# Optimization experiments

Hardware: AMD Instinct MI355X
Metric: run time of the kernel (lower is better)

The kernel has to match this reference:

```python
import jax, jax.numpy as jnp
import numpy as np
import math

N, CI, H, W, D = 8, 64, 64, 64, 64  # batch, input_dim, spatial, d_model


def setup_inputs() -> dict:
    key = jax.random.key(0)
    ks = jax.random.split(key, 6)
    s = 0.05
    return {
        "h": jax.random.normal(ks[0], (N, CI, H, W), jnp.float32),
        "m": jax.random.normal(ks[1], (N, CI, H, W), jnp.float32),
        # conv_h: 1x1, input_dim -> 3*d_model
        "Wh": jax.random.normal(ks[2], (3 * D, CI), jnp.float32) * s,
        "bh": jnp.zeros((3 * D,), jnp.float32),
        # conv_m: 1x1, input_dim -> 2*d_model
        "Wm": jax.random.normal(ks[3], (2 * D, CI), jnp.float32) * s,
        "bm": jnp.zeros((2 * D,), jnp.float32),
        # conv_z: 1x1, 2*d_model -> d_model
        "Wz": jax.random.normal(ks[4], (D, 2 * D), jnp.float32) * s,
        "bz": jnp.zeros((D,), jnp.float32),
        # conv_output: 3x3, input_dim + d_model -> 3*input_dim
        "Wo": jax.random.normal(ks[5], (3 * CI, CI + D, 3, 3), jnp.float32) * s,
        "bo": jnp.zeros((3 * CI,), jnp.float32),
    }


def _conv1x1(x, Wt, b):
    # x: (N,C,H,W), Wt: (O,C)
    return jnp.einsum('nchw,oc->nohw', x, Wt) + b[None, :, None, None]


def _attn(q, k, v):
    # q,k,v: (N,C,S); softmax over key positions
    C = q.shape[1]
    scores = jnp.einsum('ncs,nct->nst', q, k) / math.sqrt(C)  # (N,S,S)
    a = jax.nn.softmax(scores, axis=-1)
    return jnp.einsum('nst,nct->ncs', a, v)  # (N,C,S)


def reference(h, m, Wh, bh, Wm, bm, Wz, bz, Wo, bo):
    n, _, hh, ww = h.shape
    hq, hk, hv = jnp.split(_conv1x1(h, Wh, bh), 3, axis=1)
    mk, mv = jnp.split(_conv1x1(m, Wm, bm), 2, axis=1)
    flat = lambda x: x.reshape(n, D, hh * ww)
    Zh = _attn(flat(hq), flat(hk), flat(hv))
    Zm = _attn(flat(hq), flat(mk), flat(mv))
    Zcat = jnp.concatenate([Zh.reshape(n, D, hh, ww), Zm.reshape(n, D, hh, ww)], axis=1)
    Z = _conv1x1(Zcat, Wz, bz)
    x = jnp.concatenate([Z, h], axis=1)  # (N, CI+D, H, W)
    y = jax.lax.conv_general_dilated(
        x, Wo, window_strides=(1, 1), padding='SAME',
        dimension_numbers=('NCHW', 'OIHW', 'NCHW')) + bo[None, :, None, None]
    i, g, o = jnp.split(y, 3, axis=1)
    i = jax.nn.sigmoid(i)
    g = jnp.tanh(g)
    m_next = i * g + (1.0 - i) * m
    h_next = jax.nn.sigmoid(o) * m_next
    return (h_next, m_next)
```

## Files before the change

### kernel.cpp

```cpp
#include <hip/hip_runtime.h>
#include <hip/hip_bf16.h>
#include <math.h>

typedef __attribute__((ext_vector_type(8))) short bf16x8;
typedef __attribute__((ext_vector_type(4))) float f32x4;

#define DEVI __device__ __forceinline__

DEVI unsigned short f2bf(float f) {
  unsigned int u = __builtin_bit_cast(unsigned int, f);
  unsigned int r = (u + 0x7fffu + ((u >> 16) & 1u)) >> 16;
  return (unsigned short)r;
}
DEVI float bf2f(unsigned int h) {
  unsigned int u = (h & 0xffffu) << 16;
  return __builtin_bit_cast(float, u);
}
DEVI float exp2v(float x) {
  float r;
  asm("v_exp_f32 %0, %1" : "=v"(r) : "v"(x));
  return r;
}

__global__ __launch_bounds__(256) void k_prep_wo(const float* __restrict__ Wo,
                                                 unsigned short* __restrict__ wo_t) {
  int i = blockIdx.x * 256 + threadIdx.x;
  if (i >= 9 * 192 * 128) return;
  int c = i & 127;
  int rem = i >> 7;
  int o = rem % 192;
  int dydx = rem / 192;
  wo_t[i] = f2bf(Wo[(o * 128 + c) * 9 + dydx]);
}

__global__ __launch_bounds__(256) void k_prep_h(const float* __restrict__ h,
                                                unsigned short* __restrict__ xcat) {
  int i = blockIdx.x * 256 + threadIdx.x;
  int base = i * 4;
  int n = base >> 18;
  int r = base & 262143;
  int c = r >> 12;
  int s = r & 4095;
  float4 v = *(const float4*)(h + base);
  unsigned short tmp[4] = {f2bf(v.x), f2bf(v.y), f2bf(v.z), f2bf(v.w)};
  *(unsigned long long*)(xcat + (((size_t)n * 128 + 64 + c) << 12) + s) =
      *(const unsigned long long*)tmp;
}

__global__ __launch_bounds__(256) void k_proj(
    const float* __restrict__ h, const float* __restrict__ m,
    const float* __restrict__ Wh, const float* __restrict__ bh,
    const float* __restrict__ Wm, const float* __restrict__ bm,
    unsigned short* __restrict__ qb, unsigned short* __restrict__ kb,
    unsigned short* __restrict__ kmb, unsigned short* __restrict__ vb,
    unsigned short* __restrict__ vmb) {
  __shared__ float xt[64][32];
  __shared__ float wt[64][68];
  const int t = threadIdx.x;
  const int st0 = blockIdx.x * 32;
  const int n = blockIdx.y;
  const int ob = blockIdx.z;
  const float* __restrict__ x = (ob < 3) ? h : m;
  const float* __restrict__ W = (ob < 3) ? Wh : Wm;
  const float* __restrict__ bias = (ob < 3) ? bh : bm;
  const int obase = (ob < 3) ? ob * 64 : (ob - 3) * 64;

  {
    const int s = t & 31, cq = t >> 5;
    const float* src = x + (((size_t)n * 64) << 12) + st0 + s;
    #pragma unroll
    for (int r = 0; r < 8; ++r) { int c = cq + 8 * r; xt[c][s] = src[(size_t)c << 12]; }
  }
  {
    const int c = t & 63, oq = t >> 6;
    #pragma unroll
    for (int r = 0; r < 16; ++r) {
      int o = oq + 4 * r;
      wt[c][o] = W[(size_t)(obase + o) * 64 + c];
    }
  }
  __syncthreads();

  if (ob == 0 || ob == 1 || ob == 3) {
    const int og = t & 7, s = t >> 3;
    float acc[8];
    #pragma unroll
    for (int k = 0; k < 8; ++k) acc[k] = bias[obase + og * 8 + k];
    for (int c = 0; c < 64; ++c) {
      const float xv = xt[c][s];
      const float4 wa = *(const float4*)&wt[c][og * 8];
      const float4 wb = *(const float4*)&wt[c][og * 8 + 4];
      acc[0] += wa.x * xv; acc[1] += wa.y * xv; acc[2] += wa.z * xv; acc[3] += wa.w * xv;
      acc[4] += wb.x * xv; acc[5] += wb.y * xv; acc[6] += wb.z * xv; acc[7] += wb.w * xv;
    }
    const float scale = (ob == 0) ? 0.125f * 1.44269504088896340736f : 1.0f;
    unsigned short* dst = (ob == 0) ? qb : (ob == 1 ? kb : kmb);
    unsigned short tmp[8];
    #pragma unroll
    for (int k = 0; k < 8; ++k) tmp[k] = f2bf(acc[k] * scale);
    *(uint4*)(dst + (((size_t)n * 4096 + st0 + s) << 6) + og * 8) = *(const uint4*)tmp;
  } else {
    const int o = t & 63, sg = t >> 6;
    float acc[8];
    const float bv = bias[obase + o];
    #pragma unroll
    for (int k = 0; k < 8; ++k) acc[k] = bv;
    for (int c = 0; c < 64; ++c) {
      const float wv = wt[c][o];
      #pragma unroll
      for (int u = 0; u < 8; ++u) acc[u] += wv * xt[c][sg * 8 + u];
    }
    unsigned short* dst = (ob == 2) ? vb : vmb;
    unsigned short tmp[8];
    #pragma unroll
    for (int k = 0; k < 8; ++k) tmp[k] = f2bf(acc[k]);
    *(uint4*)(dst + (((size_t)n * 64 + o) << 12) + st0 + sg * 8) = *(const uint4*)tmp;
  }
}

__global__ __launch_bounds__(256) void k_attn(
    const unsigned short* __restrict__ qb, const unsigned short* __restrict__ kb,
    const unsigned short* __restrict__ kmb, const unsigned short* __restrict__ vb,
    const unsigned short* __restrict__ vmb, unsigned short* __restrict__ zcat) {
  __shared__ unsigned short Pl[4][2048];
  const int t = threadIdx.x;
  const int w = t >> 6, l = t & 63;
  const int lg = l >> 4, ll = l & 15;
  const int qt = blockIdx.x, n = blockIdx.y, sel = blockIdx.z;
  const unsigned short* __restrict__ Ksrc = sel ? kmb : kb;
  const unsigned short* __restrict__ Vsrc = sel ? vmb : vb;

  const int qbase = qt * 128 + w * 32;
  bf16x8 qfA0, qfA1, qfB0, qfB1;
  {
    const unsigned short* qp = qb + (((size_t)n * 4096 + qbase + ll) << 6) + lg * 8;
    qfA0 = *(const bf16x8*)(qp);
    qfA1 = *(const bf16x8*)(qp + 32);
    qfB0 = *(const bf16x8*)(qp + 1024);
    qfB1 = *(const bf16x8*)(qp + 1056);
  }
  f32x4 OA[4], OB[4];
  #pragma unroll
  for (int ct = 0; ct < 4; ++ct)
    #pragma unroll
    for (int e = 0; e < 4; ++e) { OA[ct][e] = 0.f; OB[ct][e] = 0.f; }
  float lsA = 0.f, lsB = 0.f;

  const unsigned short* kp = Ksrc + ((size_t)n << 18) + ((size_t)ll << 6) + lg * 8;
  const unsigned short* vp = Vsrc + ((size_t)n << 18) + ((size_t)ll << 12) + lg * 8;
  char* PlB = (char*)&Pl[w][0];
  const int swz = (ll & 7) << 4;
  const int wb = ll * 128 + lg * 8;
  const int rb = ll * 128 + lg * 16;

  for (int kt = 0; kt < 64; ++kt) {
    bf16x8 kf[8], vf[8];
    #pragma unroll
    for (int ct = 0; ct < 4; ++ct) {
      #pragma unroll
      for (int k2 = 0; k2 < 2; ++k2) {
        kf[ct * 2 + k2] = *(const bf16x8*)(kp + kt * 4096 + ct * 1024 + k2 * 32);
        vf[ct * 2 + k2] = *(const bf16x8*)(vp + (ct << 16) + kt * 64 + k2 * 32);
      }
    }
    f32x4 scA[4], scB[4];
    #pragma unroll
    for (int ct = 0; ct < 4; ++ct)
      #pragma unroll
      for (int e = 0; e < 4; ++e) { scA[ct][e] = 0.f; scB[ct][e] = 0.f; }
    #pragma unroll
    for (int k2 = 0; k2 < 2; ++k2) {
      #pragma unroll
      for (int ct = 0; ct < 4; ++ct) {
        scA[ct] = __builtin_amdgcn_mfma_f32_16x16x32_bf16(kf[ct * 2 + k2],
                      k2 ? qfA1 : qfA0, scA[ct], 0, 0, 0);
        scB[ct] = __builtin_amdgcn_mfma_f32_16x16x32_bf16(kf[ct * 2 + k2],
                      k2 ? qfB1 : qfB0, scB[ct], 0, 0, 0);
      }
    }
    #pragma unroll
    for (int ct = 0; ct < 4; ++ct) {
      float a0 = exp2v(scA[ct][0]), a1 = exp2v(scA[ct][1]);
      float a2 = exp2v(scA[ct][2]), a3 = exp2v(scA[ct][3]);
      lsA += (a0 + a1) + (a2 + a3);
      unsigned int u0, u1;
      asm("v_cvt_pk_bf16_f32 %0, %1, %2" : "=v"(u0) : "v"(a0), "v"(a1));
      asm("v_cvt_pk_bf16_f32 %0, %1, %2" : "=v"(u1) : "v"(a2), "v"(a3));
      uint2 prA; prA.x = u0; prA.y = u1;
      *(uint2*)(PlB + ((wb + ct * 32) ^ swz)) = prA;
      float b0 = exp2v(scB[ct][0]), b1 = exp2v(scB[ct][1]);
      float b2 = exp2v(scB[ct][2]), b3 = exp2v(scB[ct][3]);
      lsB += (b0 + b1) + (b2 + b3);
      unsigned int u2, u3;
      asm("v_cvt_pk_bf16_f32 %0, %1, %2" : "=v"(u2) : "v"(b0), "v"(b1));
      asm("v_cvt_pk_bf16_f32 %0, %1, %2" : "=v"(u3) : "v"(b2), "v"(b3));
      uint2 prB; prB.x = u2; prB.y = u3;
      *(uint2*)(PlB + 2048 + ((wb + ct * 32) ^ swz)) = prB;
    }
    bf16x8 pa0 = *(const bf16x8*)(PlB + (rb ^ swz));
    bf16x8 pa1 = *(const bf16x8*)(PlB + ((rb + 64) ^ swz));
    bf16x8 pb0 = *(const bf16x8*)(PlB + 2048 + (rb ^ swz));
    bf16x8 pb1 = *(const bf16x8*)(PlB + 2048 + ((rb + 64) ^ swz));
    #pragma unroll
    for (int k2 = 0; k2 < 2; ++k2) {
      #pragma unroll
      for (int ct = 0; ct < 4; ++ct) {
        OA[ct] = __builtin_amdgcn_mfma_f32_16x16x32_bf16(k2 ? pa1 : pa0,
                     vf[ct * 2 + k2], OA[ct], 0, 0, 0);
        OB[ct] = __builtin_amdgcn_mfma_f32_16x16x32_bf16(k2 ? pb1 : pb0,
                     vf[ct * 2 + k2], OB[ct], 0, 0, 0);
      }
    }
  }
  lsA += __shfl_xor(lsA, 16); lsA += __shfl_xor(lsA, 32);
  lsB += __shfl_xor(lsB, 16); lsB += __shfl_xor(lsB, 32);
  #pragma unroll
  for (int r = 0; r < 4; ++r) {
    const float liA = 1.f / __shfl(lsA, lg * 4 + r);
    const float liB = 1.f / __shfl(lsB, lg * 4 + r);
    const int rowA = qbase + lg * 4 + r;
    #pragma unroll
    for (int ct = 0; ct < 4; ++ct) {
      const int c = sel * 64 + ct * 16 + ll;
      zcat[(((size_t)n * 4096 + rowA) << 7) + c] = f2bf(OA[ct][r] * liA);
      zcat[(((size_t)n * 4096 + rowA + 16) << 7) + c] = f2bf(OB[ct][r] * liB);
    }
  }
}

__global__ __launch_bounds__(256) void k_zgemm(
    const unsigned short* __restrict__ zcat, const float* __restrict__ Wz,
    const float* __restrict__ bz, unsigned short* __restrict__ xcat) {
  __shared__ float zt[32][132];
  __shared__ float wzt[128][68];
  const int t = threadIdx.x;
  const int st0 = blockIdx.x * 32, n = blockIdx.y;
  {
    #pragma unroll
    for (int r = 0; r < 2; ++r) {
      const int chunk = t + 256 * r;
      const int s = chunk >> 4, kp = chunk & 15;
      const uint4 d = *(const uint4*)(zcat + (((size_t)n * 4096 + st0 + s) << 7) + kp * 8);
      const unsigned int u[4] = {d.x, d.y, d.z, d.w};
      #pragma unroll
      for (int e = 0; e < 4; ++e) {
        zt[s][kp * 8 + 2 * e]     = bf2f(u[e]);
        zt[s][kp * 8 + 2 * e + 1] = bf2f(u[e] >> 16);
      }
    }
  }
  {
    const int k = t & 127, czq = t >> 7;
    #pragma unroll
    for (int r = 0; r < 32; ++r) {
      const int cz = czq + 2 * r;
      wzt[k][cz] = Wz[((size_t)cz << 7) + k];
    }
  }
  __syncthreads();
  const int cz = t & 63, sg = t >> 6;
  float acc[8];
  const float bv = bz[cz];
  #pragma unroll
  for (int u = 0; u < 8; ++u) acc[u] = bv;
  for (int k = 0; k < 128; ++k) {
    const float wv = wzt[k][cz];
    #pragma unroll
    for (int u = 0; u < 8; ++u) acc[u] += wv * zt[sg * 8 + u][k];
  }
  unsigned short tmp[8];
  #pragma unroll
  for (int u = 0; u < 8; ++u) tmp[u] = f2bf(acc[u]);
  *(uint4*)(xcat + (((size_t)n * 128 + cz) << 12) + st0 + sg * 8) = *(const uint4*)tmp;
}

__global__ __launch_bounds__(256) void k_conv(
    const unsigned short* __restrict__ xcat, const unsigned short* __restrict__ wo_t,
    const float* __restrict__ bo, const float* __restrict__ m_in,
    float* __restrict__ out) {
  __shared__ unsigned short xt[3][66][40];
  const int t = threadIdx.x;
  const int wv = t >> 6, l = t & 63, lg = l >> 4, ll = l & 15;
  const int y = blockIdx.x, n = blockIdx.y;
  f32x4 acc[3][4];
  #pragma unroll
  for (int ot = 0; ot < 3; ++ot)
    #pragma unroll
    for (int ct = 0; ct < 4; ++ct)
      #pragma unroll
      for (int e = 0; e < 4; ++e) acc[ot][ct][e] = 0.f;

  for (int cb = 0; cb < 4; ++cb) {
    __syncthreads();
    {
      if (t < 192) {
        const int side = t / 96, rr = t % 96;
        xt[rr >> 5][side * 65][rr & 31] = 0;
      }
      const int wx = t & 63, q = t >> 6;
      #pragma unroll
      for (int r = 0; r < 24; ++r) {
        const int idx = q + 4 * r;
        const int c = idx & 31, dy = idx >> 5;
        const int yin = y + dy - 1;
        unsigned short vv = 0;
        if (yin >= 0 && yin < 64)
          vv = xcat[(((size_t)n * 128 + cb * 32 + c) << 12) + yin * 64 + wx];
        xt[dy][wx + 1][c] = vv;
      }
    }
    __syncthreads();
    #pragma unroll
    for (int dy = 0; dy < 3; ++dy) {
      #pragma unroll
      for (int dx = 0; dx < 3; ++dx) {
        bf16x8 bfr[4];
        #pragma unroll
        for (int ct = 0; ct < 4; ++ct)
          bfr[ct] = *(const bf16x8*)&xt[dy][ct * 16 + ll + dx][lg * 8];
        #pragma unroll
        for (int ot = 0; ot < 3; ++ot) {
          const int o = (wv + ot * 4) * 16 + ll;
          const bf16x8 afr = *(const bf16x8*)(wo_t +
              (((size_t)(dy * 3 + dx) * 192 + o) << 7) + cb * 32 + lg * 8);
          #pragma unroll
          for (int ct = 0; ct < 4; ++ct)
            acc[ot][ct] = __builtin_amdgcn_mfma_f32_16x16x32_bf16(afr, bfr[ct], acc[ot][ct], 0, 0, 0);
        }
      }
    }
  }
  #pragma unroll
  for (int ct = 0; ct < 4; ++ct) {
    #pragma unroll
    for (int r = 0; r < 4; ++r) {
      const int c = wv * 16 + lg * 4 + r;
      const int sx = ct * 16 + ll;
      const size_t pix = (((size_t)n * 64 + c) << 12) + y * 64 + sx;
      const float yi = acc[0][ct][r] + bo[c];
      const float yg = acc[1][ct][r] + bo[64 + c];
      const float yo = acc[2][ct][r] + bo[128 + c];
      const float iv = 1.f / (1.f + __expf(-yi));
      const float gv = tanhf(yg);
      const float ov = 1.f / (1.f + __expf(-yo));
      const float mo = m_in[pix];
      const float mn = iv * gv + (1.f - iv) * mo;
      out[pix] = ov * mn;
      out[pix + 2097152] = mn;
    }
  }
}

extern "C" void kernel_launch(void* const* d_in, const int* in_sizes, int n_in,
                              void* d_out, int out_size, void* d_ws, size_t ws_size,
                              hipStream_t stream) {
  const float* h  = (const float*)d_in[0];
  const float* m  = (const float*)d_in[1];
  const float* Wh = (const float*)d_in[2];
  const float* bh = (const float*)d_in[3];
  const float* Wm = (const float*)d_in[4];
  const float* bm = (const float*)d_in[5];
  const float* Wz = (const float*)d_in[6];
  const float* bz = (const float*)d_in[7];
  const float* Wo = (const float*)d_in[8];
  const float* bo = (const float*)d_in[9];
  float* out = (float*)d_out;

  unsigned short* ws  = (unsigned short*)d_ws;
  unsigned short* qbf  = ws;
  unsigned short* kbf  = qbf + 2097152;
  unsigned short* kmbf = kbf + 2097152;
  unsigned short* vbf  = kmbf + 2097152;
  unsigned short* vmbf = vbf + 2097152;
  unsigned short* zcat = vmbf + 2097152;
  unsigned short* xcat = zcat + 4194304;
  unsigned short* wot  = xcat + 4194304;

  hipLaunchKernelGGL(k_prep_wo, dim3(864), dim3(256), 0, stream, Wo, wot);
  hipLaunchKernelGGL(k_prep_h, dim3(2048), dim3(256), 0, stream, h, xcat);
  hipLaunchKernelGGL(k_proj, dim3(128, 8, 5), dim3(256), 0, stream,
                     h, m, Wh, bh, Wm, bm, qbf, kbf, kmbf, vbf, vmbf);
  hipLaunchKernelGGL(k_attn, dim3(32, 8, 2), dim3(256), 0, stream,
                     qbf, kbf, kmbf, vbf, vmbf, zcat);
  hipLaunchKernelGGL(k_zgemm, dim3(128, 8), dim3(256), 0, stream, zcat, Wz, bz, xcat);
  hipLaunchKernelGGL(k_conv, dim3(64, 8), dim3(256), 0, stream, xcat, wot, bo, m, out);
}
```

Baseline: 421.7 us.

## Split attention work to 16 query rows per wave with 512-thread blocks

```diff
diff --git a/kernel.cpp b/kernel.cpp
--- a/kernel.cpp
+++ b/kernel.cpp
@@ -118,33 +118,35 @@
   }
 }
 
-__global__ __launch_bounds__(256) void k_attn(
+__global__ __launch_bounds__(512, 4) void k_attn(
     const unsigned short* __restrict__ qb, const unsigned short* __restrict__ kb,
     const unsigned short* __restrict__ kmb, const unsigned short* __restrict__ vb,
     const unsigned short* __restrict__ vmb, unsigned short* __restrict__ zcat) {
-  __shared__ unsigned short Pl[4][2048];
+  __shared__ unsigned short Pl[8][1024];
   const int t = threadIdx.x;
   const int w = t >> 6, l = t & 63;
   const int lg = l >> 4, ll = l & 15;
-  const int qt = blockIdx.x, n = blockIdx.y, sel = blockIdx.z;
+  const int bid = blockIdx.x;
+  const int n = bid & 7;
+  const int r0 = bid >> 3;
+  const int sel = r0 & 1;
+  const int qt = r0 >> 1;
   const unsigned short* __restrict__ Ksrc = sel ? kmb : kb;
   const unsigned short* __restrict__ Vsrc = sel ? vmb : vb;
 
-  const int qbase = qt * 128 + w * 32;
-  bf16x8 qfA0, qfA1, qfB0, qfB1;
+  const int qbase = qt * 128 + w * 16;
+  bf16x8 qf0, qf1;
   {
     const unsigned short* qp = qb + (((size_t)n * 4096 + qbase + ll) << 6) + lg * 8;
-    qfA0 = *(const bf16x8*)(qp);
-    qfA1 = *(const bf16x8*)(qp + 32);
-    qfB0 = *(const bf16x8*)(qp + 1024);
-    qfB1 = *(const bf16x8*)(qp + 1056);
-  }
-  f32x4 OA[4], OB[4];
+    qf0 = *(const bf16x8*)(qp);
+    qf1 = *(const bf16x8*)(qp + 32);
+  }
+  f32x4 OA[4];
   #pragma unroll
   for (int ct = 0; ct < 4; ++ct)
     #pragma unroll
-    for (int e = 0; e < 4; ++e) { OA[ct][e] = 0.f; OB[ct][e] = 0.f; }
-  float lsA = 0.f, lsB = 0.f;
+    for (int e = 0; e < 4; ++e) OA[ct][e] = 0.f;
+  float lsA = 0.f;
 
   const unsigned short* kp = Ksrc + ((size_t)n << 18) + ((size_t)ll << 6) + lg * 8;
   const unsigned short* vp = Vsrc + ((size_t)n << 18) + ((size_t)ll << 12) + lg * 8;
@@ -163,67 +165,50 @@
         vf[ct * 2 + k2] = *(const bf16x8*)(vp + (ct << 16) + kt * 64 + k2 * 32);
       }
     }
-    f32x4 scA[4], scB[4];
+    f32x4 sc[4];
     #pragma unroll
     for (int ct = 0; ct < 4; ++ct)
       #pragma unroll
-      for (int e = 0; e < 4; ++e) { scA[ct][e] = 0.f; scB[ct][e] = 0.f; }
+      for (int e = 0; e < 4; ++e) sc[ct][e] = 0.f;
     #pragma unroll
     for (int k2 = 0; k2 < 2; ++k2) {
       #pragma unroll
       for (int ct = 0; ct < 4; ++ct) {
-        scA[ct] = __builtin_amdgcn_mfma_f32_16x16x32_bf16(kf[ct * 2 + k2],
-                      k2 ? qfA1 : qfA0, scA[ct], 0, 0, 0);
-        scB[ct] = __builtin_amdgcn_mfma_f32_16x16x32_bf16(kf[ct * 2 + k2],
-                      k2 ? qfB1 : qfB0, scB[ct], 0, 0, 0);
+        sc[ct] = __builtin_amdgcn_mfma_f32_16x16x32_bf16(kf[ct * 2 + k2],
+                     k2 ? qf1 : qf0, sc[ct], 0, 0, 0);
       }
     }
     #pragma unroll
     for (int ct = 0; ct < 4; ++ct) {
-      float a0 = exp2v(scA[ct][0]), a1 = exp2v(scA[ct][1]);
-      float a2 = exp2v(scA[ct][2]), a3 = exp2v(scA[ct][3]);
+      float a0 = exp2v(sc[ct][0]), a1 = exp2v(sc[ct][1]);
+      float a2 = exp2v(sc[ct][2]), a3 = exp2v(sc[ct][3]);
       lsA += (a0 + a1) + (a2 + a3);
       unsigned int u0, u1;
       asm("v_cvt_pk_bf16_f32 %0, %1, %2" : "=v"(u0) : "v"(a0), "v"(a1));
       asm("v_cvt_pk_bf16_f32 %0, %1, %2" : "=v"(u1) : "v"(a2), "v"(a3));
-      uint2 prA; prA.x = u0; prA.y = u1;
-      *(uint2*)(PlB + ((wb + ct * 32) ^ swz)) = prA;
-      float b0 = exp2v(scB[ct][0]), b1 = exp2v(scB[ct][1]);
-      float b2 = exp2v(scB[ct][2]), b3 = exp2v(scB[ct][3]);
-      lsB += (b0 + b1) + (b2 + b3);
-      unsigned int u2, u3;
-      asm("v_cvt_pk_bf16_f32 %0, %1, %2" : "=v"(u2) : "v"(b0), "v"(b1));
-      asm("v_cvt_pk_bf16_f32 %0, %1, %2" : "=v"(u3) : "v"(b2), "v"(b3));
-      uint2 prB; prB.x = u2; prB.y = u3;
-      *(uint2*)(PlB + 2048 + ((wb + ct * 32) ^ swz)) = prB;
+      uint2 pr; pr.x = u0; pr.y = u1;
+      *(uint2*)(PlB + ((wb + ct * 32) ^ swz)) = pr;
     }
     bf16x8 pa0 = *(const bf16x8*)(PlB + (rb ^ swz));
     bf16x8 pa1 = *(const bf16x8*)(PlB + ((rb + 64) ^ swz));
-    bf16x8 pb0 = *(const bf16x8*)(PlB + 2048 + (rb ^ swz));
-    bf16x8 pb1 = *(const bf16x8*)(PlB + 2048 + ((rb + 64) ^ swz));
     #pragma unroll
     for (int k2 = 0; k2 < 2; ++k2) {
       #pragma unroll
       for (int ct = 0; ct < 4; ++ct) {
         OA[ct] = __builtin_amdgcn_mfma_f32_16x16x32_bf16(k2 ? pa1 : pa0,
                      vf[ct * 2 + k2], OA[ct], 0, 0, 0);
-        OB[ct] = __builtin_amdgcn_mfma_f32_16x16x32_bf16(k2 ? pb1 : pb0,
-                     vf[ct * 2 + k2], OB[ct], 0, 0, 0);
       }
     }
   }
   lsA += __shfl_xor(lsA, 16); lsA += __shfl_xor(lsA, 32);
-  lsB += __shfl_xor(lsB, 16); lsB += __shfl_xor(lsB, 32);
   #pragma unroll
   for (int r = 0; r < 4; ++r) {
     const float liA = 1.f / __shfl(lsA, lg * 4 + r);
-    const float liB = 1.f / __shfl(lsB, lg * 4 + r);
     const int rowA = qbase + lg * 4 + r;
     #pragma unroll
     for (int ct = 0; ct < 4; ++ct) {
       const int c = sel * 64 + ct * 16 + ll;
       zcat[(((size_t)n * 4096 + rowA) << 7) + c] = f2bf(OA[ct][r] * liA);
-      zcat[(((size_t)n * 4096 + rowA + 16) << 7) + c] = f2bf(OB[ct][r] * liB);
     }
   }
 }
@@ -380,7 +365,7 @@
   hipLaunchKernelGGL(k_prep_h, dim3(2048), dim3(256), 0, stream, h, xcat);
   hipLaunchKernelGGL(k_proj, dim3(128, 8, 5), dim3(256), 0, stream,
                      h, m, Wh, bh, Wm, bm, qbf, kbf, kmbf, vbf, vmbf);
-  hipLaunchKernelGGL(k_attn, dim3(32, 8, 2), dim3(256), 0, stream,
+  hipLaunchKernelGGL(k_attn, dim3(512), dim3(512), 0, stream,
                      qbf, kbf, kmbf, vbf, vmbf, zcat);
   hipLaunchKernelGGL(k_zgemm, dim3(128, 8), dim3(256), 0, stream, zcat, Wz, bz, xcat);
   hipLaunchKernelGGL(k_conv, dim3(64, 8), dim3(256), 0, stream, xcat, wot, bo, m, out);
```

Result: slower. 641.1 us (+52.0%).
